# Performance work log

Hardware: AMD Instinct MI355X
Metric: run time of the kernel (lower is better)

The kernel has to match this reference:

```python
import jax, jax.numpy as jnp
import numpy as np

A, Q, D, V = 64, 32, 180, 128  # n_queries, query_len, doc_len, embed_dim
B = 2 * A                      # in-batch passages (pos + neg)


def setup_inputs() -> dict:
    key = jax.random.key(0)
    kq, kp = jax.random.split(key)
    q = jax.random.normal(kq, (A, Q, V), dtype=jnp.float32)
    p = jax.random.normal(kp, (B, D, V), dtype=jnp.float32)
    return {"q": q, "p": p}


def reference(q, p):
    # in_batch_score (multi representation, cosine/dot interaction):
    # full query-passage interaction tensor [a, b, q, d]
    term_relevance = jnp.einsum('aqv,bdv->abqd', q, p)
    # term_relevance_to_final: maxsim over doc tokens, sum over query tokens
    query_maxsim = jnp.max(term_relevance, axis=-1)   # [a, b, q]
    relevance = jnp.sum(query_maxsim, axis=-1)        # [a, b]
    return term_relevance, query_maxsim, relevance
```

## Files before the change

### kernel.cpp

```cpp
#include <hip/hip_runtime.h>
#include <hip/hip_bf16.h>

#define A_N 64
#define B_N 128
#define Q_N 32
#define D_N 180
#define V_N 128

typedef __attribute__((ext_vector_type(8))) short bf16x8;
typedef __attribute__((ext_vector_type(4))) float f32x4;

__device__ __forceinline__ short f2bf(float f) {
  __hip_bfloat16 h = __float2bfloat16(f);
  return (short)__builtin_bit_cast(unsigned short, h);
}

__device__ __forceinline__ bf16x8 pack8(const f32x4& lo, const f32x4& hi) {
  bf16x8 v;
  v[0] = f2bf(lo[0]); v[1] = f2bf(lo[1]); v[2] = f2bf(lo[2]); v[3] = f2bf(lo[3]);
  v[4] = f2bf(hi[0]); v[5] = f2bf(hi[1]); v[6] = f2bf(hi[2]); v[7] = f2bf(hi[3]);
  return v;
}

__device__ __forceinline__ void lds_fence() {
  asm volatile("s_waitcnt lgkmcnt(0)" ::: "memory");
  __builtin_amdgcn_sched_barrier(0);
}

__global__ __launch_bounds__(512, 2) void score_kernel(
    const float* __restrict__ q, const float* __restrict__ p,
    float* __restrict__ out) {
  const int bid  = blockIdx.x;
  const int b    = bid & (B_N - 1);
  const int ag   = bid >> 7;
  const int tid  = threadIdx.x;
  const int wv   = tid >> 6;
  const int lane = tid & 63;
  const int l16  = lane & 15;
  const int g    = lane >> 4;

  const float* __restrict__ pb = p + (size_t)b * D_N * V_N;

  __shared__ ushort plds[D_N * V_N];
  __shared__ __align__(16) float cbuf[8][16 * D_N];
  for (int c = tid; c < D_N * (V_N / 8); c += 512) {
    const int r  = c >> 4;
    const int s  = c & 15;
    const int sp = (s & 8) | ((s & 7) ^ (r & 7));
    const float* src = pb + (size_t)r * V_N + s * 8;
    *reinterpret_cast<bf16x8*>(&plds[r * V_N + sp * 8]) =
        pack8(*reinterpret_cast<const f32x4*>(src),
              *reinterpret_cast<const f32x4*>(src + 4));
  }

  bf16x8 qf[2][2][4];
#pragma unroll
  for (int j = 0; j < 2; ++j) {
    const int a = ag * 16 + j * 8 + wv;
    const float* __restrict__ qa = q + (size_t)a * Q_N * V_N;
#pragma unroll
    for (int qt = 0; qt < 2; ++qt)
#pragma unroll
      for (int kk = 0; kk < 4; ++kk) {
        const float* s = qa + (size_t)(qt * 16 + l16) * V_N + kk * 32 + g * 8;
        qf[j][qt][kk] = pack8(*reinterpret_cast<const f32x4*>(s),
                              *reinterpret_cast<const f32x4*>(s + 4));
      }
  }

  __syncthreads();

  float* cw = cbuf[wv];
  const size_t TERM_SZ = (size_t)A_N * B_N * Q_N * D_N;
  const size_t MS_SZ   = (size_t)A_N * B_N * Q_N;

#pragma unroll
  for (int j = 0; j < 2; ++j) {
    const int a = ag * 16 + j * 8 + wv;

    f32x4 acc[2][12];
#pragma unroll
    for (int qt = 0; qt < 2; ++qt)
#pragma unroll
      for (int dt = 0; dt < 12; ++dt)
        acc[qt][dt] = (f32x4){0.f, 0.f, 0.f, 0.f};

#pragma unroll
    for (int dt = 0; dt < 12; ++dt) {
      const int drow = dt * 16 + l16;
      const int dr   = drow < D_N ? drow : (D_N - 1);

      bf16x8 pf[4];
#pragma unroll
      for (int kk = 0; kk < 4; ++kk) {
        const int s  = kk * 4 + g;
        const int sp = (s & 8) | ((s & 7) ^ (dr & 7));
        pf[kk] = *reinterpret_cast<const bf16x8*>(&plds[dr * V_N + sp * 8]);
      }
#pragma unroll
      for (int kk = 0; kk < 4; ++kk) {
        acc[0][dt] = __builtin_amdgcn_mfma_f32_16x16x32_bf16(pf[kk], qf[j][0][kk], acc[0][dt], 0, 0, 0);
        acc[1][dt] = __builtin_amdgcn_mfma_f32_16x16x32_bf16(pf[kk], qf[j][1][kk], acc[1][dt], 0, 0, 0);
      }
    }

    float qm[2] = {-INFINITY, -INFINITY};
#pragma unroll
    for (int qt = 0; qt < 2; ++qt)
#pragma unroll
      for (int dt = 0; dt < 12; ++dt)
        qm[qt] = fmaxf(qm[qt], fmaxf(fmaxf(acc[qt][dt][0], acc[qt][dt][1]),
                                     fmaxf(acc[qt][dt][2], acc[qt][dt][3])));

    const size_t outb = ((size_t)a * B_N + b) * (size_t)(Q_N * D_N);
#pragma unroll
    for (int qt = 0; qt < 2; ++qt) {
#pragma unroll
      for (int dt = 0; dt < 12; ++dt) {
        if (dt < 11 || g == 0)
          *reinterpret_cast<f32x4*>(&cw[l16 * D_N + dt * 16 + g * 4]) = acc[qt][dt];
      }
      lds_fence();

#pragma unroll
      for (int c = 0; c < 12; ++c) {
        const int off = c * 256 + lane * 4;
        if (c < 11 || lane < 16) {
          f32x4 v = *reinterpret_cast<const f32x4*>(&cw[off]);
          *reinterpret_cast<f32x4*>(out + outb + (size_t)qt * 16 * D_N + off) = v;
        }
      }
      lds_fence();
    }

    float qm0 = qm[0], qm1 = qm[1];
    qm0 = fmaxf(qm0, __shfl_xor(qm0, 16, 64));
    qm0 = fmaxf(qm0, __shfl_xor(qm0, 32, 64));
    qm1 = fmaxf(qm1, __shfl_xor(qm1, 16, 64));
    qm1 = fmaxf(qm1, __shfl_xor(qm1, 32, 64));

    if (lane < 16) {
      float* ms = out + TERM_SZ + ((size_t)a * B_N + b) * Q_N;
      ms[lane]      = qm0;
      ms[16 + lane] = qm1;
    }

    float s = qm0 + qm1;
    s += __shfl_xor(s, 1, 64);
    s += __shfl_xor(s, 2, 64);
    s += __shfl_xor(s, 4, 64);
    s += __shfl_xor(s, 8, 64);
    if (lane == 0)
      out[TERM_SZ + MS_SZ + (size_t)a * B_N + b] = s;
  }
}

extern "C" void kernel_launch(void* const* d_in, const int* in_sizes, int n_in,
                              void* d_out, int out_size, void* d_ws, size_t ws_size,
                              hipStream_t stream) {
  const float* q = (const float*)d_in[0];
  const float* p = (const float*)d_in[1];
  float* out = (float*)d_out;
  dim3 grid(512);
  dim3 block(512);
  hipLaunchKernelGGL(score_kernel, grid, block, 0, stream, q, p, out);
}
```

Before: 53.71 us.

## Double query tiles per block and prefetch next query fragments

Each block now processes 32 queries against one passage instead of 16, halving the grid and the number of times each passage is loaded and converted into LDS. Query fragments for the next iteration are loaded into a second register buffer during the current iteration's epilogue. The trade-off is fewer resident blocks per CU (one per CU) and more registers, which may reduce latency hiding for the large output stores.

```diff
diff --git a/kernel.cpp b/kernel.cpp
--- a/kernel.cpp
+++ b/kernel.cpp
@@ -54,19 +54,20 @@
   }
 
   bf16x8 qf[2][2][4];
-#pragma unroll
-  for (int j = 0; j < 2; ++j) {
-    const int a = ag * 16 + j * 8 + wv;
-    const float* __restrict__ qa = q + (size_t)a * Q_N * V_N;
-#pragma unroll
-    for (int qt = 0; qt < 2; ++qt)
-#pragma unroll
-      for (int kk = 0; kk < 4; ++kk) {
-        const float* s = qa + (size_t)(qt * 16 + l16) * V_N + kk * 32 + g * 8;
-        qf[j][qt][kk] = pack8(*reinterpret_cast<const f32x4*>(s),
-                              *reinterpret_cast<const f32x4*>(s + 4));
-      }
+#define LOADQF(buf, jj)                                                       \
+  {                                                                           \
+    const int aq = ag * 32 + (jj) * 8 + wv;                                   \
+    const float* __restrict__ qa = q + (size_t)aq * Q_N * V_N;                \
+    _Pragma("unroll")                                                         \
+    for (int qt = 0; qt < 2; ++qt)                                            \
+      _Pragma("unroll")                                                       \
+      for (int kk = 0; kk < 4; ++kk) {                                        \
+        const float* s = qa + (size_t)(qt * 16 + l16) * V_N + kk * 32 + g * 8;\
+        qf[buf][qt][kk] = pack8(*reinterpret_cast<const f32x4*>(s),          \
+                                *reinterpret_cast<const f32x4*>(s + 4));     \
+      }                                                                       \
   }
+  LOADQF(0, 0);
 
   __syncthreads();
 
@@ -75,8 +76,9 @@
   const size_t MS_SZ   = (size_t)A_N * B_N * Q_N;
 
 #pragma unroll
-  for (int j = 0; j < 2; ++j) {
-    const int a = ag * 16 + j * 8 + wv;
+  for (int j = 0; j < 4; ++j) {
+    const int a  = ag * 32 + j * 8 + wv;
+    const int jb = j & 1;
 
     f32x4 acc[2][12];
 #pragma unroll
@@ -99,10 +101,12 @@
       }
 #pragma unroll
       for (int kk = 0; kk < 4; ++kk) {
-        acc[0][dt] = __builtin_amdgcn_mfma_f32_16x16x32_bf16(pf[kk], qf[j][0][kk], acc[0][dt], 0, 0, 0);
-        acc[1][dt] = __builtin_amdgcn_mfma_f32_16x16x32_bf16(pf[kk], qf[j][1][kk], acc[1][dt], 0, 0, 0);
+        acc[0][dt] = __builtin_amdgcn_mfma_f32_16x16x32_bf16(pf[kk], qf[jb][0][kk], acc[0][dt], 0, 0, 0);
+        acc[1][dt] = __builtin_amdgcn_mfma_f32_16x16x32_bf16(pf[kk], qf[jb][1][kk], acc[1][dt], 0, 0, 0);
       }
     }
+
+    if (j < 3) LOADQF(!jb ? 1 : 0, j + 1);
 
     float qm[2] = {-INFINITY, -INFINITY};
 #pragma unroll
@@ -153,6 +157,7 @@
     if (lane == 0)
       out[TERM_SZ + MS_SZ + (size_t)a * B_N + b] = s;
   }
+#undef LOADQF
 }
 
 extern "C" void kernel_launch(void* const* d_in, const int* in_sizes, int n_in,
@@ -161,7 +166,7 @@
   const float* q = (const float*)d_in[0];
   const float* p = (const float*)d_in[1];
   float* out = (float*)d_out;
-  dim3 grid(512);
+  dim3 grid(256);
   dim3 block(512);
   hipLaunchKernelGGL(score_kernel, grid, block, 0, stream, q, p, out);
 }
```

New measurement: 43.00 us (median of 2 runs). 1.25x faster.
